# Performance work log

Hardware: AMD Instinct MI355X
Metric: run time of the kernel (lower is better)

Reference implementation:

```python
import jax, jax.numpy as jnp
import numpy as np

# dims: batch, seqlen, d_model, d_inner=2*d_model, d_state, dt_rank=ceil(dm/16), n_layer, vocab, d_conv
B_, L_, DM, DI, N, RK, NL, V, K = 2, 2048, 512, 1024, 16, 32, 4, 32000, 4


def setup_inputs() -> dict:
    key = jax.random.key(0)
    ks = jax.random.split(key, 10)
    s = lambda k, shape, scale: jax.random.normal(k, shape, jnp.float32) * scale
    return {
        "input_ids": jax.random.randint(ks[0], (B_, L_), 0, V),
        "emb": s(ks[1], (V, DM), 0.02),
        "in_proj_w": s(ks[2], (NL, 2 * DI, DM), DM ** -0.5),
        "conv_w": s(ks[3], (NL, DI, K), 0.2),
        "conv_b": jnp.zeros((NL, DI), jnp.float32),
        "x_proj_w": s(ks[4], (NL, RK + 2 * N, DI), DI ** -0.5),
        "dt_proj_w": s(ks[5], (NL, DI, RK), RK ** -0.5),
        "dt_proj_b": jnp.full((NL, DI), -4.6, jnp.float32),  # softplus^-1(~0.01)
        "A_log": jnp.tile(jnp.log(jnp.arange(1, N + 1, dtype=jnp.float32))[None, None, :], (NL, DI, 1)),
        "Dp": jnp.ones((NL, DI), jnp.float32),
        "out_proj_w": s(ks[6], (NL, DM, DI), DI ** -0.5),
        "norm_w": jnp.ones((NL, DM), jnp.float32),
        "norm_b": jnp.zeros((NL, DM), jnp.float32),
        "normf_w": jnp.ones((DM,), jnp.float32),
        "normf_b": jnp.zeros((DM,), jnp.float32),
        "dec_w": s(ks[7], (V, DM), DM ** -0.5),
        "dec_b": jnp.zeros((V,), jnp.float32),
    }


def layer_norm(x, w, b, eps=1e-5):
    m = x.mean(-1, keepdims=True)
    v = ((x - m) ** 2).mean(-1, keepdims=True)
    return (x - m) * jax.lax.rsqrt(v + eps) * w + b


def mamba_mixer(x, iw, cw, cb, xw, dw, db, A_log, Dv, ow):
    B, L, _ = x.shape
    xz = x @ iw.T                      # [B,L,2*DI]
    u, z = jnp.split(xz, 2, -1)
    # depthwise causal conv1d, kernel K
    up = jnp.pad(u, ((0, 0), (K - 1, 0), (0, 0)))
    u = sum(up[:, k:k + L, :] * cw[:, k] for k in range(K)) + cb
    u = jax.nn.silu(u)
    xdbl = u @ xw.T                    # [B,L,RK+2N]
    dt, Bm, Cm = jnp.split(xdbl, [RK, RK + N], -1)
    dt = jax.nn.softplus(dt @ dw.T + db)   # [B,L,DI]
    A = -jnp.exp(A_log)                    # [DI,N]
    dA = jnp.exp(dt[..., None] * A)                              # [B,L,DI,N]
    dBu = dt[..., None] * Bm[:, :, None, :] * u[..., None]       # [B,L,DI,N]

    def step(h, inp):
        dA_t, dBu_t, C_t = inp
        h = dA_t * h + dBu_t
        return h, jnp.einsum('bdn,bn->bd', h, C_t)

    h0 = jnp.zeros((B, DI, N), x.dtype)
    _, ys = jax.lax.scan(step, h0, (dA.transpose(1, 0, 2, 3), dBu.transpose(1, 0, 2, 3), Cm.transpose(1, 0, 2)))
    y = ys.transpose(1, 0, 2) + u * Dv
    y = y * jax.nn.silu(z)
    return y @ ow.T


def reference(input_ids, emb, in_proj_w, conv_w, conv_b, x_proj_w, dt_proj_w, dt_proj_b,
              A_log, Dp, out_proj_w, norm_w, norm_b, normf_w, normf_b, dec_w, dec_b):
    h = emb[input_ids]                 # [B,L,DM]
    residual = None
    for i in range(NL):
        residual = h + residual if residual is not None else h
        hn = layer_norm(residual, norm_w[i], norm_b[i])
        h = mamba_mixer(hn, in_proj_w[i], conv_w[i], conv_b[i], x_proj_w[i],
                        dt_proj_w[i], dt_proj_b[i], A_log[i], Dp[i], out_proj_w[i])
    residual = h + residual
    h = layer_norm(residual, normf_w, normf_b)
    return h @ dec_w.T + dec_b         # [B,L,V]
```

## Files before the change

### kernel.cpp

```cpp
#include <hip/hip_runtime.h>
#include <cstdint>
#include <cstddef>

typedef unsigned short u16;
typedef __attribute__((ext_vector_type(8))) short short8;
typedef __attribute__((ext_vector_type(4))) float f32x4;
typedef __attribute__((ext_vector_type(4))) unsigned short us4;

#define NB 2
#define SEQ 2048
#define DMODEL 512
#define DINNER 1024
#define NSTATE 16
#define RKK 32
#define NLAYER 4
#define VOCAB 32000
#define MROWS 4096
#define NCHUNK 64
#define LCHUNK 32
#define XP_SPLITK 8
#define XP_KCH 128

#define GLOAD16(gp, lp) __builtin_amdgcn_global_load_lds( \
    (const __attribute__((address_space(1))) void*)(gp),  \
    (__attribute__((address_space(3))) void*)(lp), 16, 0, 0)

static __device__ __forceinline__ u16 f2bf(float f) {
  union { float f; uint32_t u; } v; v.f = f;
  uint32_t r = (v.u + 0x7FFFu + ((v.u >> 16) & 1u)) >> 16;
  return (u16)r;
}
static __device__ __forceinline__ float bf2f(u16 x) {
  union { uint32_t u; float f; } v; v.u = ((uint32_t)x) << 16; return v.f;
}

__global__ __launch_bounds__(256) void cvt_all_k(
    const float* __restrict__ ipw, const float* __restrict__ dtw,
    const float* __restrict__ opw, const float* __restrict__ dw,
    u16* __restrict__ w_in, u16* __restrict__ w_dt,
    u16* __restrict__ w_out, u16* __restrict__ w_dec) {
  const long n0 = (long)NLAYER * 2 * DINNER * DMODEL / 4;
  const long n1 = (long)NLAYER * DINNER * RKK / 4;
  const long n2 = (long)NLAYER * DMODEL * DINNER / 4;
  const long n3 = (long)VOCAB * DMODEL / 4;
  long i = (long)blockIdx.x * 256 + threadIdx.x;
  const float* s; u16* d; long off;
  if (i < n0) { s = ipw; d = w_in; off = i; }
  else if (i < n0 + n1) { s = dtw; d = w_dt; off = i - n0; }
  else if (i < n0 + n1 + n2) { s = opw; d = w_out; off = i - n0 - n1; }
  else if (i < n0 + n1 + n2 + n3) { s = dw; d = w_dec; off = i - n0 - n1 - n2; }
  else return;
  f32x4 v = *(const f32x4*)(s + off * 4);
  us4 o; o.x = f2bf(v.x); o.y = f2bf(v.y); o.z = f2bf(v.z); o.w = f2bf(v.w);
  *(us4*)(d + off * 4) = o;
}
__global__ __launch_bounds__(256) void cvt_xproj_k(const float* __restrict__ s, u16* __restrict__ d) {
  long i = (long)blockIdx.x * 256 + threadIdx.x;
  int c = (int)(i & 1023); int r = ((int)(i >> 10)) & 127; int l = (int)(i >> 17);
  d[i] = (r < 64) ? f2bf(s[((long)l * 64 + r) * 1024 + c]) : (u16)0;
}

template <int MODE>
__global__ __launch_bounds__(256) void ln_k(const int* __restrict__ ids, const float* __restrict__ emb,
                                            float* __restrict__ resid, const float* __restrict__ hadd,
                                            const float* __restrict__ w, const float* __restrict__ b,
                                            u16* __restrict__ obf) {
  int m = blockIdx.x, t = threadIdx.x;
  long base = (long)m * DMODEL;
  float x0, x1;
  if (MODE == 0) {
    long ebase = (long)ids[m] * DMODEL;
    x0 = emb[ebase + t]; x1 = emb[ebase + t + 256];
    resid[base + t] = x0; resid[base + t + 256] = x1;
  } else {
    x0 = resid[base + t] + hadd[base + t];
    x1 = resid[base + t + 256] + hadd[base + t + 256];
    resid[base + t] = x0; resid[base + t + 256] = x1;
  }
  float s = x0 + x1, q = x0 * x0 + x1 * x1;
  #pragma unroll
  for (int o = 1; o < 64; o <<= 1) { s += __shfl_xor(s, o, 64); q += __shfl_xor(q, o, 64); }
  __shared__ float ss[4], qq[4];
  int wv = t >> 6;
  if ((t & 63) == 0) { ss[wv] = s; qq[wv] = q; }
  __syncthreads();
  s = ss[0] + ss[1] + ss[2] + ss[3];
  q = qq[0] + qq[1] + qq[2] + qq[3];
  float mean = s * (1.f / DMODEL);
  float var = q * (1.f / DMODEL) - mean * mean;
  float rs = rsqrtf(var + 1e-5f);
  obf[base + t]       = f2bf((x0 - mean) * rs * w[t] + b[t]);
  obf[base + t + 256] = f2bf((x1 - mean) * rs * w[t + 256] + b[t + 256]);
}

__global__ __launch_bounds__(256) void conv_silu_k(const u16* __restrict__ xzb, const float* __restrict__ cw,
                            const float* __restrict__ cb, u16* __restrict__ ub) {
  int tid = blockIdx.x * 256 + threadIdx.x;
  int d = tid & (DINNER - 1);
  int g = tid >> 10;
  int m0 = g << 2;
  int t0 = m0 & (SEQ - 1);
  float w0 = cw[d * 4 + 0], w1 = cw[d * 4 + 1], w2 = cw[d * 4 + 2], w3 = cw[d * 4 + 3];
  float bias = cb[d];
  float v[7];
  #pragma unroll
  for (int j = 0; j < 7; ++j) {
    int tt = t0 + j - 3;
    v[j] = (tt >= 0) ? bf2f(xzb[(long)(m0 + j - 3) * (2 * DINNER) + d]) : 0.f;
  }
  #pragma unroll
  for (int i = 0; i < 4; ++i) {
    float acc = bias + v[i] * w0 + v[i + 1] * w1 + v[i + 2] * w2 + v[i + 3] * w3;
    float sv = acc / (1.f + __expf(-acc));
    ub[(long)(m0 + i) * DINNER + d] = f2bf(sv);
  }
}

template <int EPI, int BK, bool SPLIT>
__global__ __launch_bounds__(256) void gemm_bf16(
    const u16* __restrict__ A, int lda, const u16* __restrict__ W, int ldw,
    float* __restrict__ C, u16* __restrict__ Cb, int ldc,
    const float* __restrict__ bias, int K, int kchunk, long zstride) {
  const int tid = threadIdx.x;
  const int nwg = gridDim.x * gridDim.y;
  const int wgid = blockIdx.y * gridDim.x + blockIdx.x;
  const int q = nwg >> 3;
  const int swz = (wgid & 7) * q + (wgid >> 3);
  const int bn = swz % gridDim.x, bm = swz / gridDim.x;
  int kb = 0, ke = K;
  if (SPLIT) { kb = blockIdx.z * kchunk; ke = kb + kchunk; C += (long)blockIdx.z * zstride; }
  const int wave = tid >> 6, lane = tid & 63;
  const int wm = (wave >> 1) * 64, wn = (wave & 1) * 64;
  __shared__ __align__(16) u16 sA[128 * BK];
  __shared__ __align__(16) u16 sB[128 * BK];
  f32x4 acc[4][4] = {};
  const long arow0 = (long)bm * 128, brow0 = (long)bn * 128;
  const int frow = lane & 15, fk = (lane >> 4) << 3;
  for (int k0 = kb; k0 < ke; k0 += BK) {
    __syncthreads();
    if (BK == 32) {
      const int srow = lane >> 2, scol = (lane & 3) << 3;
      #pragma unroll
      for (int i = 0; i < 2; ++i) {
        int c = wave * 2 + i;
        GLOAD16(A + (arow0 + 16 * c + srow) * (long)lda + k0 + scol, sA + c * 512);
        GLOAD16(W + (brow0 + 16 * c + srow) * (long)ldw + k0 + scol, sB + c * 512);
      }
    } else {
      const int srow = lane >> 3, scol = (lane & 7) << 3;
      #pragma unroll
      for (int i = 0; i < 4; ++i) {
        int c = wave * 4 + i;
        GLOAD16(A + (arow0 + 8 * c + srow) * (long)lda + k0 + scol, sA + c * 512);
        GLOAD16(W + (brow0 + 8 * c + srow) * (long)ldw + k0 + scol, sB + c * 512);
      }
    }
    asm volatile("s_waitcnt vmcnt(0)" ::: "memory");
    __syncthreads();
    #pragma unroll
    for (int ks = 0; ks < BK / 32; ++ks) {
      short8 aF[4], bF[4];
      #pragma unroll
      for (int i = 0; i < 4; ++i) aF[i] = *(const short8*)(sA + (wm + i * 16 + frow) * BK + ks * 32 + fk);
      #pragma unroll
      for (int i = 0; i < 4; ++i) bF[i] = *(const short8*)(sB + (wn + i * 16 + frow) * BK + ks * 32 + fk);
      #pragma unroll
      for (int mi = 0; mi < 4; ++mi)
        #pragma unroll
        for (int ni = 0; ni < 4; ++ni)
          acc[mi][ni] = __builtin_amdgcn_mfma_f32_16x16x32_bf16(aF[mi], bF[ni], acc[mi][ni], 0, 0, 0);
    }
  }
  const int ccol = lane & 15, crow = (lane >> 4) << 2;
  #pragma unroll
  for (int mi = 0; mi < 4; ++mi) {
    #pragma unroll
    for (int ni = 0; ni < 4; ++ni) {
      long gr0 = arow0 + wm + mi * 16 + crow;
      long gc = brow0 + wn + ni * 16 + ccol;
      #pragma unroll
      for (int r = 0; r < 4; ++r) {
        float v = acc[mi][ni][r];
        long idx = (gr0 + r) * (long)ldc + gc;
        if (EPI == 0) {
          C[idx] = v;
        } else if (EPI == 1) {
          Cb[idx] = f2bf(v);
        } else if (EPI == 2) {
          float x = v + bias[gc];
          Cb[idx] = f2bf((x > 20.f) ? x : log1pf(__expf(x)));
        } else {
          __builtin_nontemporal_store(v + bias[gc], &C[idx]);
        }
      }
    }
  }
}

__global__ __launch_bounds__(256) void xp_comb_k(const float* __restrict__ P, float* __restrict__ xd,
                          u16* __restrict__ xdb) {
  long i = (long)blockIdx.x * 256 + threadIdx.x;
  float s = 0.f;
  #pragma unroll
  for (int z = 0; z < XP_SPLITK; ++z) s += P[(long)z * MROWS * 128 + i];
  xd[i] = s; xdb[i] = f2bf(s);
}

__global__ __launch_bounds__(256) void scanA_k(const u16* __restrict__ dtb, const u16* __restrict__ ubf,
                        const float* __restrict__ xd, const float* __restrict__ alog_l,
                        float* __restrict__ P, float* __restrict__ S) {
  int bid = blockIdx.x;
  int tid = threadIdx.x;
  int b = bid >> 8;
  int c = (bid >> 2) & (NCHUNK - 1);
  int d = ((bid & 3) << 8) + tid;
  long rbase = (long)(b * SEQ + c * LCHUNK);
  __shared__ __align__(16) float sB[LCHUNK][NSTATE];
  if (tid < 128) {
    int t = tid >> 2, k4 = (tid & 3) << 2;
    *(f32x4*)&sB[t][k4] = *(const f32x4*)(xd + (rbase + t) * 128 + RKK + k4);
  }
  u16 dtv[LCHUNK], uv[LCHUNK];
  const u16* dp = dtb + rbase * DINNER + d;
  const u16* up = ubf + rbase * DINNER + d;
  #pragma unroll
  for (int tt = 0; tt < LCHUNK; ++tt) { dtv[tt] = dp[(long)tt * DINNER]; uv[tt] = up[(long)tt * DINNER]; }
  float A[NSTATE], h[NSTATE], p[NSTATE];
  #pragma unroll
  for (int n4 = 0; n4 < 4; ++n4) {
    f32x4 a4 = *(const f32x4*)(alog_l + d * NSTATE + n4 * 4);
    #pragma unroll
    for (int j = 0; j < 4; ++j) { A[n4 * 4 + j] = -__expf(a4[j]); h[n4 * 4 + j] = 0.f; p[n4 * 4 + j] = 1.f; }
  }
  __syncthreads();
  #pragma unroll
  for (int tt = 0; tt < LCHUNK; ++tt) {
    float dv = bf2f(dtv[tt]);
    float du = dv * bf2f(uv[tt]);
    f32x4 b0 = *(const f32x4*)&sB[tt][0], b1 = *(const f32x4*)&sB[tt][4];
    f32x4 b2 = *(const f32x4*)&sB[tt][8], b3 = *(const f32x4*)&sB[tt][12];
    #pragma unroll
    for (int n = 0; n < NSTATE; ++n) {
      float dA = __expf(dv * A[n]);
      float bx = (n < 4) ? b0[n & 3] : (n < 8) ? b1[n & 3] : (n < 12) ? b2[n & 3] : b3[n & 3];
      h[n] = dA * h[n] + du * bx;
      p[n] *= dA;
    }
  }
  long base = (((long)(b * DINNER + d)) * NCHUNK + c) * NSTATE;
  #pragma unroll
  for (int n4 = 0; n4 < 4; ++n4) {
    f32x4 pv, sv;
    #pragma unroll
    for (int j = 0; j < 4; ++j) { pv[j] = p[n4 * 4 + j]; sv[j] = h[n4 * 4 + j]; }
    *(f32x4*)(P + base + n4 * 4) = pv;
    *(f32x4*)(S + base + n4 * 4) = sv;
  }
}

__global__ __launch_bounds__(256) void scanB_k(const float* __restrict__ P, const float* __restrict__ S,
                        float* __restrict__ Hin) {
  int w = blockIdx.x * 4 + (threadIdx.x >> 6);
  int lane = threadIdx.x & 63;
  long base = ((long)w * NCHUNK + lane) * NSTATE;
  float p[NSTATE], s[NSTATE];
  #pragma unroll
  for (int n = 0; n < NSTATE; ++n) { p[n] = P[base + n]; s[n] = S[base + n]; }
  #pragma unroll
  for (int off = 1; off < 64; off <<= 1) {
    float pp[NSTATE], sp[NSTATE];
    #pragma unroll
    for (int n = 0; n < NSTATE; ++n) {
      pp[n] = __shfl_up(p[n], off, 64);
      sp[n] = __shfl_up(s[n], off, 64);
    }
    if (lane >= off) {
      #pragma unroll
      for (int n = 0; n < NSTATE; ++n) { s[n] = p[n] * sp[n] + s[n]; p[n] *= pp[n]; }
    }
  }
  #pragma unroll
  for (int n = 0; n < NSTATE; ++n) {
    float hv = __shfl_up(s[n], 1, 64);
    Hin[base + n] = (lane == 0) ? 0.f : hv;
  }
}

__global__ __launch_bounds__(256) void scanC_k(const u16* __restrict__ dtb, const u16* __restrict__ ubf,
                        const float* __restrict__ xd, const float* __restrict__ alog_l,
                        const float* __restrict__ Dp_l, const u16* __restrict__ xzb,
                        const float* __restrict__ Hin, u16* __restrict__ ybf) {
  int bid = blockIdx.x;
  int tid = threadIdx.x;
  int b = bid >> 8;
  int c = (bid >> 2) & (NCHUNK - 1);
  int d = ((bid & 3) << 8) + tid;
  long rbase = (long)(b * SEQ + c * LCHUNK);
  __shared__ __align__(16) float sBC[LCHUNK][2 * NSTATE];
  {
    int t = tid >> 3, k4 = (tid & 7) << 2;
    *(f32x4*)&sBC[t][k4] = *(const f32x4*)(xd + (rbase + t) * 128 + RKK + k4);
  }
  u16 dtv[LCHUNK], uv[LCHUNK], zv[LCHUNK];
  const u16* dp = dtb + rbase * DINNER + d;
  const u16* up = ubf + rbase * DINNER + d;
  const u16* zp = xzb + rbase * (2 * DINNER) + DINNER + d;
  #pragma unroll
  for (int tt = 0; tt < LCHUNK; ++tt) {
    dtv[tt] = dp[(long)tt * DINNER]; uv[tt] = up[(long)tt * DINNER];
    zv[tt] = zp[(long)tt * 2 * DINNER];
  }
  float A[NSTATE], h[NSTATE];
  long hbase = (((long)(b * DINNER + d)) * NCHUNK + c) * NSTATE;
  #pragma unroll
  for (int n4 = 0; n4 < 4; ++n4) {
    f32x4 a4 = *(const f32x4*)(alog_l + d * NSTATE + n4 * 4);
    f32x4 h4 = *(const f32x4*)(Hin + hbase + n4 * 4);
    #pragma unroll
    for (int j = 0; j < 4; ++j) { A[n4 * 4 + j] = -__expf(a4[j]); h[n4 * 4 + j] = h4[j]; }
  }
  float Dv = Dp_l[d];
  u16* yp = ybf + rbase * DINNER + d;
  __syncthreads();
  #pragma unroll
  for (int tt = 0; tt < LCHUNK; ++tt) {
    float dv = bf2f(dtv[tt]);
    float uvf = bf2f(uv[tt]);
    float du = dv * uvf;
    f32x4 b0 = *(const f32x4*)&sBC[tt][0], b1 = *(const f32x4*)&sBC[tt][4];
    f32x4 b2 = *(const f32x4*)&sBC[tt][8], b3 = *(const f32x4*)&sBC[tt][12];
    f32x4 c0 = *(const f32x4*)&sBC[tt][16], c1 = *(const f32x4*)&sBC[tt][20];
    f32x4 c2 = *(const f32x4*)&sBC[tt][24], c3 = *(const f32x4*)&sBC[tt][28];
    float y = 0.f;
    #pragma unroll
    for (int n = 0; n < NSTATE; ++n) {
      float dA = __expf(dv * A[n]);
      float bx = (n < 4) ? b0[n & 3] : (n < 8) ? b1[n & 3] : (n < 12) ? b2[n & 3] : b3[n & 3];
      float cx = (n < 4) ? c0[n & 3] : (n < 8) ? c1[n & 3] : (n < 12) ? c2[n & 3] : c3[n & 3];
      h[n] = dA * h[n] + du * bx;
      y += h[n] * cx;
    }
    y += uvf * Dv;
    float z = bf2f(zv[tt]);
    y *= z / (1.f + __expf(-z));
    yp[(long)tt * DINNER] = f2bf(y);
  }
}

extern "C" void kernel_launch(void* const* d_in, const int* in_sizes, int n_in,
                              void* d_out, int out_size, void* d_ws, size_t ws_size,
                              hipStream_t stream) {
  (void)in_sizes; (void)n_in; (void)out_size; (void)ws_size;
  const int*   ids = (const int*)d_in[0];
  const float* emb = (const float*)d_in[1];
  const float* ipw = (const float*)d_in[2];
  const float* cw  = (const float*)d_in[3];
  const float* cb  = (const float*)d_in[4];
  const float* xpw = (const float*)d_in[5];
  const float* dtw = (const float*)d_in[6];
  const float* dtb = (const float*)d_in[7];
  const float* alg = (const float*)d_in[8];
  const float* Dpp = (const float*)d_in[9];
  const float* opw = (const float*)d_in[10];
  const float* nw  = (const float*)d_in[11];
  const float* nb  = (const float*)d_in[12];
  const float* nfw = (const float*)d_in[13];
  const float* nfb = (const float*)d_in[14];
  const float* dw  = (const float*)d_in[15];
  const float* db  = (const float*)d_in[16];

  char* p = (char*)d_ws;
  auto carve = [&](size_t bytes) { void* r = (void*)p; p += (bytes + 255) & ~(size_t)255; return r; };
  float* resid  = (float*)carve((size_t)MROWS * DMODEL * 4);
  float* hmix   = (float*)carve((size_t)MROWS * DMODEL * 4);
  u16*   hnbf   = (u16*)  carve((size_t)MROWS * DMODEL * 2);
  u16*   hfbf   = (u16*)  carve((size_t)MROWS * DMODEL * 2);
  u16*   xzb    = (u16*)  carve((size_t)MROWS * 2 * DINNER * 2);
  u16*   ubf    = (u16*)  carve((size_t)MROWS * DINNER * 2);
  float* xdbl   = (float*)carve((size_t)MROWS * 128 * 4);
  u16*   xdblbf = (u16*)  carve((size_t)MROWS * 128 * 2);
  float* xdP    = (float*)carve((size_t)XP_SPLITK * MROWS * 128 * 4);
  u16*   dtb16  = (u16*)  carve((size_t)MROWS * DINNER * 2);
  u16*   ybf    = (u16*)  carve((size_t)MROWS * DINNER * 2);
  float* chkP   = (float*)carve((size_t)NB * DINNER * NCHUNK * NSTATE * 4);
  float* chkS   = (float*)carve((size_t)NB * DINNER * NCHUNK * NSTATE * 4);
  float* hin    = (float*)carve((size_t)NB * DINNER * NCHUNK * NSTATE * 4);
  u16*   w_in   = (u16*)carve((size_t)NLAYER * 2 * DINNER * DMODEL * 2);
  u16*   w_xp   = (u16*)carve((size_t)NLAYER * 128 * DINNER * 2);
  u16*   w_dt   = (u16*)carve((size_t)NLAYER * DINNER * RKK * 2);
  u16*   w_out  = (u16*)carve((size_t)NLAYER * DMODEL * DINNER * 2);
  u16*   w_dec  = (u16*)carve((size_t)VOCAB * DMODEL * 2);

  {
    long nv4 = ((long)NLAYER * 2 * DINNER * DMODEL + (long)NLAYER * DINNER * RKK +
                (long)NLAYER * DMODEL * DINNER + (long)VOCAB * DMODEL) / 4;
    cvt_all_k<<<(int)((nv4 + 255) / 256), 256, 0, stream>>>(ipw, dtw, opw, dw, w_in, w_dt, w_out, w_dec);
    cvt_xproj_k<<<(NLAYER * 128 * DINNER) / 256, 256, 0, stream>>>(xpw, w_xp);
  }

  for (int i = 0; i < NLAYER; ++i) {
    if (i == 0)
      ln_k<0><<<MROWS, 256, 0, stream>>>(ids, emb, resid, nullptr, nw, nb, hnbf);
    else
      ln_k<1><<<MROWS, 256, 0, stream>>>(nullptr, nullptr, resid, hmix, nw + i * DMODEL, nb + i * DMODEL, hnbf);
    gemm_bf16<1, 64, false><<<dim3(2 * DINNER / 128, MROWS / 128), 256, 0, stream>>>(
        hnbf, DMODEL, w_in + (long)i * 2 * DINNER * DMODEL, DMODEL,
        nullptr, xzb, 2 * DINNER, nullptr, DMODEL, 0, 0);
    conv_silu_k<<<(MROWS / 4 * DINNER) / 256, 256, 0, stream>>>(
        xzb, cw + (long)i * DINNER * 4, cb + i * DINNER, ubf);
    gemm_bf16<0, 64, true><<<dim3(1, MROWS / 128, XP_SPLITK), 256, 0, stream>>>(
        ubf, DINNER, w_xp + (long)i * 128 * DINNER, DINNER,
        xdP, nullptr, 128, nullptr, DINNER, XP_KCH, (long)MROWS * 128);
    xp_comb_k<<<(MROWS * 128) / 256, 256, 0, stream>>>(xdP, xdbl, xdblbf);
    gemm_bf16<2, 32, false><<<dim3(DINNER / 128, MROWS / 128), 256, 0, stream>>>(
        xdblbf, 128, w_dt + (long)i * DINNER * RKK, RKK,
        nullptr, dtb16, DINNER, dtb + i * DINNER, RKK, 0, 0);
    scanA_k<<<NB * NCHUNK * 4, 256, 0, stream>>>(
        dtb16, ubf, xdbl, alg + (long)i * DINNER * NSTATE, chkP, chkS);
    scanB_k<<<(NB * DINNER) / 4, 256, 0, stream>>>(chkP, chkS, hin);
    scanC_k<<<NB * NCHUNK * 4, 256, 0, stream>>>(
        dtb16, ubf, xdbl, alg + (long)i * DINNER * NSTATE, Dpp + i * DINNER, xzb, hin, ybf);
    gemm_bf16<0, 64, false><<<dim3(DMODEL / 128, MROWS / 128), 256, 0, stream>>>(
        ybf, DINNER, w_out + (long)i * DMODEL * DINNER, DINNER,
        hmix, nullptr, DMODEL, nullptr, DINNER, 0, 0);
  }
  ln_k<1><<<MROWS, 256, 0, stream>>>(nullptr, nullptr, resid, hmix, nfw, nfb, hfbf);
  gemm_bf16<3, 64, false><<<dim3(VOCAB / 128, MROWS / 128), 256, 0, stream>>>(
      hfbf, DMODEL, w_dec, DMODEL, (float*)d_out, nullptr, VOCAB, db, DMODEL, 0, 0);
}
```

Baseline: 893.4 us.

## Swizzle LDS layout, split-K out_proj, and add 256x128 decoder GEMM kernel

Applies an XOR swizzle to the BK=64 LDS tile layout so that MFMA fragment reads avoid bank conflicts. Splits the out_proj GEMM into two K halves to raise its block count, and folds the two partial sums into the following layernorm. Adds a dedicated 512-thread decoder GEMM with 256x128 tiles to improve reuse on the large vocab projection. The trade-offs are an extra partial buffer and more global traffic in the layernorm.

Result: faster. 840.3 us (-5.9%).

```diff
diff --git a/kernel.cpp b/kernel.cpp
--- a/kernel.cpp
+++ b/kernel.cpp
@@ -62,7 +62,8 @@
 
 template <int MODE>
 __global__ __launch_bounds__(256) void ln_k(const int* __restrict__ ids, const float* __restrict__ emb,
-                                            float* __restrict__ resid, const float* __restrict__ hadd,
+                                            float* __restrict__ resid, const float* __restrict__ h0,
+                                            const float* __restrict__ h1,
                                             const float* __restrict__ w, const float* __restrict__ b,
                                             u16* __restrict__ obf) {
   int m = blockIdx.x, t = threadIdx.x;
@@ -73,8 +74,8 @@
     x0 = emb[ebase + t]; x1 = emb[ebase + t + 256];
     resid[base + t] = x0; resid[base + t + 256] = x1;
   } else {
-    x0 = resid[base + t] + hadd[base + t];
-    x1 = resid[base + t + 256] + hadd[base + t + 256];
+    x0 = resid[base + t] + h0[base + t] + h1[base + t];
+    x1 = resid[base + t + 256] + h0[base + t + 256] + h1[base + t + 256];
     resid[base + t] = x0; resid[base + t + 256] = x1;
   }
   float s = x0 + x1, q = x0 * x0 + x1 * x1;
@@ -136,6 +137,7 @@
   f32x4 acc[4][4] = {};
   const long arow0 = (long)bm * 128, brow0 = (long)bn * 128;
   const int frow = lane & 15, fk = (lane >> 4) << 3;
+  const int rsw = (frow & 7) << 3;
   for (int k0 = kb; k0 < ke; k0 += BK) {
     __syncthreads();
     if (BK == 32) {
@@ -147,7 +149,8 @@
         GLOAD16(W + (brow0 + 16 * c + srow) * (long)ldw + k0 + scol, sB + c * 512);
       }
     } else {
-      const int srow = lane >> 3, scol = (lane & 7) << 3;
+      const int srow = lane >> 3;
+      const int scol = (((lane & 7) ^ (lane >> 3)) << 3);
       #pragma unroll
       for (int i = 0; i < 4; ++i) {
         int c = wave * 4 + i;
@@ -161,9 +164,15 @@
     for (int ks = 0; ks < BK / 32; ++ks) {
       short8 aF[4], bF[4];
       #pragma unroll
-      for (int i = 0; i < 4; ++i) aF[i] = *(const short8*)(sA + (wm + i * 16 + frow) * BK + ks * 32 + fk);
-      #pragma unroll
-      for (int i = 0; i < 4; ++i) bF[i] = *(const short8*)(sB + (wn + i * 16 + frow) * BK + ks * 32 + fk);
+      for (int i = 0; i < 4; ++i) {
+        int idx = (wm + i * 16 + frow) * BK + ks * 32 + fk;
+        aF[i] = *(const short8*)(sA + (BK == 64 ? (idx ^ rsw) : idx));
+      }
+      #pragma unroll
+      for (int i = 0; i < 4; ++i) {
+        int idx = (wn + i * 16 + frow) * BK + ks * 32 + fk;
+        bF[i] = *(const short8*)(sB + (BK == 64 ? (idx ^ rsw) : idx));
+      }
       #pragma unroll
       for (int mi = 0; mi < 4; ++mi)
         #pragma unroll
@@ -193,6 +202,75 @@
           __builtin_nontemporal_store(v + bias[gc], &C[idx]);
         }
       }
+    }
+  }
+}
+
+__global__ __launch_bounds__(512) void gemm_dec(
+    const u16* __restrict__ A, const u16* __restrict__ W,
+    float* __restrict__ C, const float* __restrict__ bias) {
+  const int tid = threadIdx.x;
+  const int nwg = gridDim.x * gridDim.y;
+  const int wgid = blockIdx.y * gridDim.x + blockIdx.x;
+  const int q = nwg >> 3;
+  const int swz = (wgid & 7) * q + (wgid >> 3);
+  const int bn = swz % gridDim.x, bm = swz / gridDim.x;
+  const int wave = tid >> 6, lane = tid & 63;
+  const int wm = (wave >> 1) << 6;
+  const int wn = (wave & 1) << 6;
+  __shared__ __align__(16) u16 sA[256 * 64];
+  __shared__ __align__(16) u16 sB[128 * 64];
+  f32x4 acc[4][4] = {};
+  const long arow0 = (long)bm * 256, brow0 = (long)bn * 128;
+  const int frow = lane & 15, fk = (lane >> 4) << 3;
+  const int rsw = (frow & 7) << 3;
+  const int srow = lane >> 3;
+  const int scol = (((lane & 7) ^ (lane >> 3)) << 3);
+  for (int k0 = 0; k0 < DMODEL; k0 += 64) {
+    __syncthreads();
+    #pragma unroll
+    for (int i = 0; i < 4; ++i) {
+      int c = wave * 4 + i;
+      GLOAD16(A + (arow0 + 8 * c + srow) * (long)DMODEL + k0 + scol, sA + c * 512);
+    }
+    #pragma unroll
+    for (int i = 0; i < 2; ++i) {
+      int c = wave * 2 + i;
+      GLOAD16(W + (brow0 + 8 * c + srow) * (long)DMODEL + k0 + scol, sB + c * 512);
+    }
+    asm volatile("s_waitcnt vmcnt(0)" ::: "memory");
+    __syncthreads();
+    #pragma unroll
+    for (int ks = 0; ks < 2; ++ks) {
+      short8 aF[4], bF[4];
+      #pragma unroll
+      for (int i = 0; i < 4; ++i) {
+        int idx = (wm + i * 16 + frow) * 64 + ks * 32 + fk;
+        aF[i] = *(const short8*)(sA + (idx ^ rsw));
+      }
+      #pragma unroll
+      for (int i = 0; i < 4; ++i) {
+        int idx = (wn + i * 16 + frow) * 64 + ks * 32 + fk;
+        bF[i] = *(const short8*)(sB + (idx ^ rsw));
+      }
+      #pragma unroll
+      for (int mi = 0; mi < 4; ++mi)
+        #pragma unroll
+        for (int ni = 0; ni < 4; ++ni)
+          acc[mi][ni] = __builtin_amdgcn_mfma_f32_16x16x32_bf16(aF[mi], bF[ni], acc[mi][ni], 0, 0, 0);
+    }
+  }
+  const int ccol = lane & 15, crow = (lane >> 4) << 2;
+  #pragma unroll
+  for (int mi = 0; mi < 4; ++mi) {
+    #pragma unroll
+    for (int ni = 0; ni < 4; ++ni) {
+      long gr0 = arow0 + wm + mi * 16 + crow;
+      long gc = brow0 + wn + ni * 16 + ccol;
+      float bv = bias[gc];
+      #pragma unroll
+      for (int r = 0; r < 4; ++r)
+        __builtin_nontemporal_store(acc[mi][ni][r] + bv, &C[(gr0 + r) * (long)VOCAB + gc]);
     }
   }
 }
@@ -372,7 +450,7 @@
   char* p = (char*)d_ws;
   auto carve = [&](size_t bytes) { void* r = (void*)p; p += (bytes + 255) & ~(size_t)255; return r; };
   float* resid  = (float*)carve((size_t)MROWS * DMODEL * 4);
-  float* hmix   = (float*)carve((size_t)MROWS * DMODEL * 4);
+  float* hmixP  = (float*)carve((size_t)2 * MROWS * DMODEL * 4);
   u16*   hnbf   = (u16*)  carve((size_t)MROWS * DMODEL * 2);
   u16*   hfbf   = (u16*)  carve((size_t)MROWS * DMODEL * 2);
   u16*   xzb    = (u16*)  carve((size_t)MROWS * 2 * DINNER * 2);
@@ -400,9 +478,10 @@
 
   for (int i = 0; i < NLAYER; ++i) {
     if (i == 0)
-      ln_k<0><<<MROWS, 256, 0, stream>>>(ids, emb, resid, nullptr, nw, nb, hnbf);
+      ln_k<0><<<MROWS, 256, 0, stream>>>(ids, emb, resid, nullptr, nullptr, nw, nb, hnbf);
     else
-      ln_k<1><<<MROWS, 256, 0, stream>>>(nullptr, nullptr, resid, hmix, nw + i * DMODEL, nb + i * DMODEL, hnbf);
+      ln_k<1><<<MROWS, 256, 0, stream>>>(nullptr, nullptr, resid, hmixP, hmixP + (long)MROWS * DMODEL,
+                                         nw + i * DMODEL, nb + i * DMODEL, hnbf);
     gemm_bf16<1, 64, false><<<dim3(2 * DINNER / 128, MROWS / 128), 256, 0, stream>>>(
         hnbf, DMODEL, w_in + (long)i * 2 * DINNER * DMODEL, DMODEL,
         nullptr, xzb, 2 * DINNER, nullptr, DMODEL, 0, 0);
@@ -420,11 +499,12 @@
     scanB_k<<<(NB * DINNER) / 4, 256, 0, stream>>>(chkP, chkS, hin);
     scanC_k<<<NB * NCHUNK * 4, 256, 0, stream>>>(
         dtb16, ubf, xdbl, alg + (long)i * DINNER * NSTATE, Dpp + i * DINNER, xzb, hin, ybf);
-    gemm_bf16<0, 64, false><<<dim3(DMODEL / 128, MROWS / 128), 256, 0, stream>>>(
+    gemm_bf16<0, 64, true><<<dim3(DMODEL / 128, MROWS / 128, 2), 256, 0, stream>>>(
         ybf, DINNER, w_out + (long)i * DMODEL * DINNER, DINNER,
-        hmix, nullptr, DMODEL, nullptr, DINNER, 0, 0);
-  }
-  ln_k<1><<<MROWS, 256, 0, stream>>>(nullptr, nullptr, resid, hmix, nfw, nfb, hfbf);
-  gemm_bf16<3, 64, false><<<dim3(VOCAB / 128, MROWS / 128), 256, 0, stream>>>(
-      hfbf, DMODEL, w_dec, DMODEL, (float*)d_out, nullptr, VOCAB, db, DMODEL, 0, 0);
-}
+        hmixP, nullptr, DMODEL, nullptr, DINNER, DINNER / 2, (long)MROWS * DMODEL);
+  }
+  ln_k<1><<<MROWS, 256, 0, stream>>>(nullptr, nullptr, resid, hmixP, hmixP + (long)MROWS * DMODEL,
+                                     nfw, nfb, hfbf);
+  gemm_dec<<<dim3(VOCAB / 128, MROWS / 256), 512, 0, stream>>>(
+      hfbf, w_dec, (float*)d_out, db);
+}
```
